# Kernel optimization log

Hardware: AMD Instinct MI355X
Metric: run time of the kernel (lower is better)

The kernel has to match this reference:

```python
import jax, jax.numpy as jnp
import numpy as np

L, D, H, EXP = 6, 512, 8, 4
DH = D // H
EPS = 1e-3  # keras LayerNormalization default epsilon


def _layer_norm(x, gamma, beta):
    mu = jnp.mean(x, axis=-1, keepdims=True)
    var = jnp.mean(jnp.square(x - mu), axis=-1, keepdims=True)
    return (x - mu) * jax.lax.rsqrt(var + EPS) * gamma + beta


def setup_inputs() -> dict:
    key = jax.random.key(0)
    ks = jax.random.split(key, 10)
    B, S = 8, 1024
    s_attn = 1.0 / np.sqrt(D)
    s_ffn1 = 1.0 / np.sqrt(D)
    s_ffn2 = 1.0 / np.sqrt(D * EXP)
    return {
        "x": jax.random.normal(ks[0], (B, S, D), dtype=jnp.float32),
        "Wq": jax.random.normal(ks[1], (L, D, D), dtype=jnp.float32) * s_attn,
        "Wk": jax.random.normal(ks[2], (L, D, D), dtype=jnp.float32) * s_attn,
        "Wv": jax.random.normal(ks[3], (L, D, D), dtype=jnp.float32) * s_attn,
        "Wo": jax.random.normal(ks[4], (L, D, D), dtype=jnp.float32) * s_attn,
        "W1": jax.random.normal(ks[5], (L, D, D * EXP), dtype=jnp.float32) * s_ffn1,
        "b1": jnp.zeros((L, D * EXP), dtype=jnp.float32),
        "W2": jax.random.normal(ks[6], (L, D * EXP, D), dtype=jnp.float32) * s_ffn2,
        "b2": jnp.zeros((L, D), dtype=jnp.float32),
        "g_attn": jnp.ones((L, D), dtype=jnp.float32),
        "be_attn": jnp.zeros((L, D), dtype=jnp.float32),
        "g_ffn": jnp.ones((L, D), dtype=jnp.float32),
        "be_ffn": jnp.zeros((L, D), dtype=jnp.float32),
    }


def _self_attention(y, wq, wk, wv, wo):
    B, S, _ = y.shape
    q = (y @ wq).reshape(B, S, H, DH)
    k = (y @ wk).reshape(B, S, H, DH)
    v = (y @ wv).reshape(B, S, H, DH)
    scores = jnp.einsum("bqhd,bkhd->bhqk", q, k) / np.sqrt(float(DH))
    attn = jax.nn.softmax(scores, axis=-1)
    z = jnp.einsum("bhqk,bkhd->bqhd", attn, v).reshape(B, S, D)
    return z @ wo


def reference(x, Wq, Wk, Wv, Wo, W1, b1, W2, b2, g_attn, be_attn, g_ffn, be_ffn):
    encoded = x
    for l in range(L):
        # pre-LN self-attention + residual (dropout=identity at inference)
        attended = _layer_norm(encoded, g_attn[l], be_attn[l])
        attended = _self_attention(attended, Wq[l], Wk[l], Wv[l], Wo[l])
        attended = encoded + attended
        # pre-LN FFN + residual
        h = _layer_norm(attended, g_ffn[l], be_ffn[l])
        h = jax.nn.relu(h @ W1[l] + b1[l]) @ W2[l] + b2[l]
        encoded = attended + h
    return encoded
```

## Files before the change

### kernel.cpp

```cpp
#include <hip/hip_runtime.h>


#define SEQ 1024
#define ROWS 8192
#define QKVW 1536

using bf16x8 = __attribute__((ext_vector_type(8))) short;
using f32x4  = __attribute__((ext_vector_type(4))) float;

__device__ __forceinline__ unsigned short f2bf(float f) {
  union { float f; unsigned u; } v; v.f = f;
  unsigned r = v.u + 0x7FFFu + ((v.u >> 16) & 1u);
  return (unsigned short)(r >> 16);
}

__device__ __forceinline__ float exp2_fast(float x) {
  float r;
  asm("v_exp_f32 %0, %1" : "=v"(r) : "v"(x));
  return r;
}

__device__ __forceinline__ void gl16(const void* g, void* l) {
  typedef const unsigned int __attribute__((address_space(1)))* GP;
  typedef unsigned int __attribute__((address_space(3)))* LP;
  __builtin_amdgcn_global_load_lds((GP)g, (LP)l, 16, 0, 0);
}

__global__ __launch_bounds__(256) void transpose_cast_k(
    const float* __restrict__ W, unsigned short* __restrict__ Wt,
    int K, int N, int lstride, float scale)
{
  __shared__ float tile[32][33];
  const int l = blockIdx.z;
  const float* Wl = W + (size_t)l * K * N;
  unsigned short* Wtl = Wt + (size_t)l * lstride;
  const int k0 = blockIdx.y * 32, n0 = blockIdx.x * 32;
  const int tx = threadIdx.x & 31, ty = threadIdx.x >> 5;
  #pragma unroll
  for (int i = ty; i < 32; i += 8)
    tile[i][tx] = Wl[(size_t)(k0 + i) * N + n0 + tx];
  __syncthreads();
  #pragma unroll
  for (int i = ty; i < 32; i += 8)
    Wtl[(size_t)(n0 + i) * K + k0 + tx] = f2bf(tile[tx][i] * scale);
}

__global__ __launch_bounds__(256) void ln_k(
    const float* __restrict__ x, const float* __restrict__ g,
    const float* __restrict__ be, unsigned short* __restrict__ y, int rows)
{
  const int wid = (blockIdx.x << 2) | (threadIdx.x >> 6);
  const int lane = threadIdx.x & 63;
  if (wid >= rows) return;
  const float4* xr = reinterpret_cast<const float4*>(x + (size_t)wid * 512);
  float4 a = xr[lane];
  float4 b = xr[lane + 64];
  float s = a.x + a.y + a.z + a.w + b.x + b.y + b.z + b.w;
  #pragma unroll
  for (int m = 32; m >= 1; m >>= 1) s += __shfl_xor(s, m);
  const float mu = s * (1.0f / 512.0f);
  const float d0 = a.x - mu, d1 = a.y - mu, d2 = a.z - mu, d3 = a.w - mu;
  const float e0 = b.x - mu, e1 = b.y - mu, e2 = b.z - mu, e3 = b.w - mu;
  float q = d0*d0 + d1*d1 + d2*d2 + d3*d3 + e0*e0 + e1*e1 + e2*e2 + e3*e3;
  #pragma unroll
  for (int m = 32; m >= 1; m >>= 1) q += __shfl_xor(q, m);
  const float inv = rsqrtf(q * (1.0f / 512.0f) + 1e-3f);
  const float4* gr = reinterpret_cast<const float4*>(g);
  const float4* br = reinterpret_cast<const float4*>(be);
  const float4 g0 = gr[lane], g1 = gr[lane + 64];
  const float4 h0 = br[lane], h1 = br[lane + 64];
  ushort4 o0, o1;
  o0.x = f2bf(d0 * inv * g0.x + h0.x);
  o0.y = f2bf(d1 * inv * g0.y + h0.y);
  o0.z = f2bf(d2 * inv * g0.z + h0.z);
  o0.w = f2bf(d3 * inv * g0.w + h0.w);
  o1.x = f2bf(e0 * inv * g1.x + h1.x);
  o1.y = f2bf(e1 * inv * g1.y + h1.y);
  o1.z = f2bf(e2 * inv * g1.z + h1.z);
  o1.w = f2bf(e3 * inv * g1.w + h1.w);
  *reinterpret_cast<ushort4*>(y + (size_t)wid * 512 + lane * 4) = o0;
  *reinterpret_cast<ushort4*>(y + (size_t)wid * 512 + (lane + 64) * 4) = o1;
}

template<bool RELU, bool HASBIAS, bool HASRES, bool OUTBF>
__global__ __launch_bounds__(256) void gemm128_k(
    const unsigned short* __restrict__ A,
    const unsigned short* __restrict__ Wt,
    const float* __restrict__ bias,
    const float* __restrict__ res,
    void* __restrict__ outp, int M, int N, int K)
{
  __shared__ __align__(16) unsigned short As0[4096], Bs0[4096];
  __shared__ __align__(16) unsigned short As1[4096], Bs1[4096];
  const int t = threadIdx.x;
  const int nwg = gridDim.x * gridDim.y;
  const int bid = blockIdx.y * gridDim.x + blockIdx.x;
  const int nid = (bid & 7) * (nwg >> 3) + (bid >> 3);
  const int bx = nid % gridDim.x, by = nid / gridDim.x;
  const int m0 = by * 128, n0 = bx * 128;
  const int w = t >> 6, lane = t & 63, llo = lane & 15, lhi = lane >> 4;
  const int wr = w >> 1, wc = w & 1;

  const int sr = t >> 2, sg = (t & 3) ^ ((t >> 3) & 3);
  const unsigned short* pa = &A[(size_t)(m0 + sr) * K + sg * 8];
  const unsigned short* pb = &Wt[(size_t)(n0 + sr) * K + sg * 8];

#define GSTAGE128(AsX, BsX, koff) do { \
    gl16(pa + (koff), &AsX[t * 8]); \
    gl16(pa + (size_t)64 * K + (koff), &AsX[2048 + t * 8]); \
    gl16(pb + (koff), &BsX[t * 8]); \
    gl16(pb + (size_t)64 * K + (koff), &BsX[2048 + t * 8]); \
  } while (0)

  const int pgo = (lhi ^ ((llo >> 1) & 3)) * 8;

#define GCOMP128(AsX, BsX) do { \
    bf16x8 af[4], bfr[4]; \
    _Pragma("unroll") \
    for (int f = 0; f < 4; f++) { \
      af[f]  = *reinterpret_cast<const bf16x8*>(&AsX[(wr * 64 + f * 16 + llo) * 32 + pgo]); \
      bfr[f] = *reinterpret_cast<const bf16x8*>(&BsX[(wc * 64 + f * 16 + llo) * 32 + pgo]); \
    } \
    _Pragma("unroll") \
    for (int fi = 0; fi < 4; fi++) \
      _Pragma("unroll") \
      for (int fj = 0; fj < 4; fj++) \
        acc[fi][fj] = __builtin_amdgcn_mfma_f32_16x16x32_bf16(af[fi], bfr[fj], acc[fi][fj], 0, 0, 0); \
  } while (0)

  f32x4 acc[4][4] = {};
  GSTAGE128(As0, Bs0, 0);
  for (int k0 = 0; k0 < K; k0 += 64) {
    __syncthreads();
    GSTAGE128(As1, Bs1, k0 + 32);
    GCOMP128(As0, Bs0);
    __syncthreads();
    if (k0 + 64 < K) GSTAGE128(As0, Bs0, k0 + 64);
    GCOMP128(As1, Bs1);
  }
#undef GSTAGE128
#undef GCOMP128

  const int row0 = m0 + wr * 64, col0 = n0 + wc * 64;
  #pragma unroll
  for (int fi = 0; fi < 4; fi++)
    #pragma unroll
    for (int fj = 0; fj < 4; fj++)
      #pragma unroll
      for (int i = 0; i < 4; i++) {
        const int row = row0 + fi * 16 + lhi * 4 + i;
        const int col = col0 + fj * 16 + llo;
        float v = acc[fi][fj][i];
        if (HASBIAS) v += bias[col];
        if (HASRES)  v += res[(size_t)row * N + col];
        if (RELU)    v = fmaxf(v, 0.0f);
        if (OUTBF) ((unsigned short*)outp)[(size_t)row * N + col] = f2bf(v);
        else       ((float*)outp)[(size_t)row * N + col] = v;
      }
}

template<bool RELU, bool HASBIAS, bool HASRES, bool OUTBF>
__global__ __launch_bounds__(256) void gemm64_k(
    const unsigned short* __restrict__ A,
    const unsigned short* __restrict__ Wt,
    const float* __restrict__ bias,
    const float* __restrict__ res,
    void* __restrict__ outp, int M, int N, int K)
{
  __shared__ __align__(16) unsigned short As0[2048], Bs0[4096];
  __shared__ __align__(16) unsigned short As1[2048], Bs1[4096];
  const int t = threadIdx.x;
  const int nwg = gridDim.x * gridDim.y;
  const int bid = blockIdx.y * gridDim.x + blockIdx.x;
  const int nid = (bid & 7) * (nwg >> 3) + (bid >> 3);
  const int bx = nid % gridDim.x, by = nid / gridDim.x;
  const int m0 = by * 64, n0 = bx * 128;
  const int w = t >> 6, lane = t & 63, llo = lane & 15, lhi = lane >> 4;
  const int wr = w >> 1, wc = w & 1;

  const int sr = t >> 2, sg = (t & 3) ^ ((t >> 3) & 3);
  const unsigned short* pa = &A[(size_t)(m0 + sr) * K + sg * 8];
  const unsigned short* pb = &Wt[(size_t)(n0 + sr) * K + sg * 8];

#define GSTAGE64(AsX, BsX, koff) do { \
    gl16(pa + (koff), &AsX[t * 8]); \
    gl16(pb + (koff), &BsX[t * 8]); \
    gl16(pb + (size_t)64 * K + (koff), &BsX[2048 + t * 8]); \
  } while (0)

  const int pgo = (lhi ^ ((llo >> 1) & 3)) * 8;

#define GCOMP64(AsX, BsX) do { \
    bf16x8 af[2], bfr[4]; \
    _Pragma("unroll") \
    for (int f = 0; f < 2; f++) \
      af[f] = *reinterpret_cast<const bf16x8*>(&AsX[(wr * 32 + f * 16 + llo) * 32 + pgo]); \
    _Pragma("unroll") \
    for (int f = 0; f < 4; f++) \
      bfr[f] = *reinterpret_cast<const bf16x8*>(&BsX[(wc * 64 + f * 16 + llo) * 32 + pgo]); \
    _Pragma("unroll") \
    for (int fi = 0; fi < 2; fi++) \
      _Pragma("unroll") \
      for (int fj = 0; fj < 4; fj++) \
        acc[fi][fj] = __builtin_amdgcn_mfma_f32_16x16x32_bf16(af[fi], bfr[fj], acc[fi][fj], 0, 0, 0); \
  } while (0)

  f32x4 acc[2][4] = {};
  GSTAGE64(As0, Bs0, 0);
  for (int k0 = 0; k0 < K; k0 += 64) {
    __syncthreads();
    GSTAGE64(As1, Bs1, k0 + 32);
    GCOMP64(As0, Bs0);
    __syncthreads();
    if (k0 + 64 < K) GSTAGE64(As0, Bs0, k0 + 64);
    GCOMP64(As1, Bs1);
  }
#undef GSTAGE64
#undef GCOMP64

  const int row0 = m0 + wr * 32, col0 = n0 + wc * 64;
  #pragma unroll
  for (int fi = 0; fi < 2; fi++)
    #pragma unroll
    for (int fj = 0; fj < 4; fj++)
      #pragma unroll
      for (int i = 0; i < 4; i++) {
        const int row = row0 + fi * 16 + lhi * 4 + i;
        const int col = col0 + fj * 16 + llo;
        float v = acc[fi][fj][i];
        if (HASBIAS) v += bias[col];
        if (HASRES)  v += res[(size_t)row * N + col];
        if (RELU)    v = fmaxf(v, 0.0f);
        if (OUTBF) ((unsigned short*)outp)[(size_t)row * N + col] = f2bf(v);
        else       ((float*)outp)[(size_t)row * N + col] = v;
      }
}

__global__ __launch_bounds__(256) void vtrans_k(
    const unsigned short* __restrict__ QKV, unsigned short* __restrict__ VT)
{
  __shared__ unsigned short tile[64][66];
  const int kt = blockIdx.x, bh = blockIdx.y;
  const int bb = bh >> 3, h = bh & 7;
  const int t = threadIdx.x;
  const int r = t >> 2, c0 = (t & 3) * 16;
  const unsigned short* src = &QKV[((size_t)bb * SEQ + kt * 64 + r) * QKVW + 1024 + h * 64 + c0];
  *reinterpret_cast<uint4*>(&tile[r][c0])     = *reinterpret_cast<const uint4*>(src);
  *reinterpret_cast<uint4*>(&tile[r][c0 + 8]) = *reinterpret_cast<const uint4*>(src + 8);
  __syncthreads();
  const int dv = t >> 2, kv0 = (t & 3) * 16;
  unsigned short tmp[16];
  #pragma unroll
  for (int j = 0; j < 16; j++) tmp[j] = tile[kv0 + j][dv];
  ushort4 o0, o1, o2, o3;
  o0.x = tmp[0];  o0.y = tmp[1];  o0.z = tmp[2];  o0.w = tmp[3];
  o1.x = tmp[4];  o1.y = tmp[5];  o1.z = tmp[6];  o1.w = tmp[7];
  o2.x = tmp[8];  o2.y = tmp[9];  o2.z = tmp[10]; o2.w = tmp[11];
  o3.x = tmp[12]; o3.y = tmp[13]; o3.z = tmp[14]; o3.w = tmp[15];
  unsigned short* dst = &VT[((size_t)bh * 64 + dv) * SEQ + kt * 64 + kv0];
  *reinterpret_cast<ushort4*>(dst)      = o0;
  *reinterpret_cast<ushort4*>(dst + 4)  = o1;
  *reinterpret_cast<ushort4*>(dst + 8)  = o2;
  *reinterpret_cast<ushort4*>(dst + 12) = o3;
}

__global__ __launch_bounds__(256) void attn_k(
    const unsigned short* __restrict__ QKV,
    const unsigned short* __restrict__ VT,
    unsigned short* __restrict__ Zb)
{
  __shared__ __align__(16) unsigned short Ks0[4096], Vs0[4096];
  __shared__ __align__(16) unsigned short Ks1[4096], Vs1[4096];
  __shared__ __align__(16) unsigned short Ps[4096];

  const int t = threadIdx.x;
  const int qt = blockIdx.x, h = blockIdx.y, bb = blockIdx.z;
  const int w = t >> 6, lane = t & 63, llo = lane & 15, lhi = lane >> 4;
  const size_t rowb = (size_t)bb * SEQ;
  const int kcol = 512 + h * 64;
  const size_t vtb = (size_t)(bb * 8 + h) * 64 * SEQ;

  bf16x8 aq[2];
  #pragma unroll
  for (int ds = 0; ds < 2; ds++)
    aq[ds] = *reinterpret_cast<const bf16x8*>(
        &QKV[(rowb + qt * 64 + w * 16 + llo) * QKVW + h * 64 + ds * 32 + lhi * 8]);

  const int cA = t, cB = 256 + t;
  const int gA = cA >> 6, lA = cA & 63, gB = cB >> 6, lB = cB & 63;
  const unsigned short* kpA = &QKV[(rowb + (gA >> 1) * 16 + (lA & 15)) * QKVW + kcol + (gA & 1) * 32 + (lA >> 4) * 8];
  const unsigned short* kpB = &QKV[(rowb + (gB >> 1) * 16 + (lB & 15)) * QKVW + kcol + (gB & 1) * 32 + (lB >> 4) * 8];
  const unsigned short* vpA = &VT[vtb + (size_t)((gA >> 1) * 16 + (lA & 15)) * SEQ + (gA & 1) * 32 + (lA >> 4) * 8];
  const unsigned short* vpB = &VT[vtb + (size_t)((gB >> 1) * 16 + (lB & 15)) * SEQ + (gB & 1) * 32 + (lB >> 4) * 8];

#define ASTAGE(KsX, VsX, ktt) do { \
    gl16(kpA + (size_t)(ktt) * 64 * QKVW, &KsX[cA * 8]); \
    gl16(kpB + (size_t)(ktt) * 64 * QKVW, &KsX[cB * 8]); \
    gl16(vpA + (ktt) * 64, &VsX[cA * 8]); \
    gl16(vpB + (ktt) * 64, &VsX[cB * 8]); \
  } while (0)

#define ACOMP(KsX, VsX) do { \
    f32x4 s_[4]; \
    _Pragma("unroll") \
    for (int fj = 0; fj < 4; fj++) \
      _Pragma("unroll") \
      for (int i = 0; i < 4; i++) s_[fj][i] = -16.0f; \
    _Pragma("unroll") \
    for (int ds = 0; ds < 2; ds++) \
      _Pragma("unroll") \
      for (int fj = 0; fj < 4; fj++) { \
        bf16x8 bk = *reinterpret_cast<const bf16x8*>(&KsX[((fj * 2 + ds) * 64 + lane) * 8]); \
        s_[fj] = __builtin_amdgcn_mfma_f32_16x16x32_bf16(aq[ds], bk, s_[fj], 0, 0, 0); \
      } \
    _Pragma("unroll") \
    for (int fj = 0; fj < 4; fj++) \
      _Pragma("unroll") \
      for (int i = 0; i < 4; i++) { \
        const float p = exp2_fast(s_[fj][i]); \
        l_[i] += p; \
        Ps[w * 1024 + (fj >> 1) * 512 + ((fj & 1) * 2 + (llo >> 3)) * 128 \
           + (lhi * 4 + i) * 8 + (llo & 7)] = f2bf(p); \
      } \
    _Pragma("unroll") \
    for (int ks = 0; ks < 2; ks++) { \
      bf16x8 ap = *reinterpret_cast<const bf16x8*>(&Ps[w * 1024 + (ks * 64 + lane) * 8]); \
      _Pragma("unroll") \
      for (int fo = 0; fo < 4; fo++) { \
        bf16x8 bv = *reinterpret_cast<const bf16x8*>(&VsX[((fo * 2 + ks) * 64 + lane) * 8]); \
        o_[fo] = __builtin_amdgcn_mfma_f32_16x16x32_bf16(ap, bv, o_[fo], 0, 0, 0); \
      } \
    } \
  } while (0)

  float l_[4] = {0.0f, 0.0f, 0.0f, 0.0f};
  f32x4 o_[4] = {};

  ASTAGE(Ks0, Vs0, 0);
  for (int kt = 0; kt < 16; kt += 2) {
    __syncthreads();
    ASTAGE(Ks1, Vs1, kt + 1);
    ACOMP(Ks0, Vs0);
    __syncthreads();
    if (kt + 2 < 16) ASTAGE(Ks0, Vs0, kt + 2);
    ACOMP(Ks1, Vs1);
  }
#undef ASTAGE
#undef ACOMP

  #pragma unroll
  for (int i = 0; i < 4; i++) {
    l_[i] += __shfl_xor(l_[i], 1);
    l_[i] += __shfl_xor(l_[i], 2);
    l_[i] += __shfl_xor(l_[i], 4);
    l_[i] += __shfl_xor(l_[i], 8);
  }

  #pragma unroll
  for (int fo = 0; fo < 4; fo++)
    #pragma unroll
    for (int i = 0; i < 4; i++) {
      const float v = o_[fo][i] / l_[i];
      Zb[(rowb + qt * 64 + w * 16 + lhi * 4 + i) * 512 + h * 64 + fo * 16 + llo] = f2bf(v);
    }
}

extern "C" void kernel_launch(void* const* d_in, const int* in_sizes, int n_in,
                              void* d_out, int out_size, void* d_ws, size_t ws_size,
                              hipStream_t stream)
{
  const float* x   = (const float*)d_in[0];
  const float* Wq  = (const float*)d_in[1];
  const float* Wk  = (const float*)d_in[2];
  const float* Wv  = (const float*)d_in[3];
  const float* Wo  = (const float*)d_in[4];
  const float* W1  = (const float*)d_in[5];
  const float* b1  = (const float*)d_in[6];
  const float* W2  = (const float*)d_in[7];
  const float* b2  = (const float*)d_in[8];
  const float* ga  = (const float*)d_in[9];
  const float* ba  = (const float*)d_in[10];
  const float* gf  = (const float*)d_in[11];
  const float* bfn = (const float*)d_in[12];
  float* out = (float*)d_out;

  char* p = (char*)d_ws;
  auto alloc = [&](size_t bytes) { void* r = (void*)p; p += (bytes + 255) & ~(size_t)255; return r; };
  float* E0 = (float*)alloc((size_t)ROWS * 512 * 4);
  float* E1 = (float*)alloc((size_t)ROWS * 512 * 4);
  unsigned short* Ybf   = (unsigned short*)alloc((size_t)ROWS * 512 * 2);
  unsigned short* QKVbf = (unsigned short*)alloc((size_t)ROWS * QKVW * 2);
  unsigned short* H1bf  = (unsigned short*)alloc((size_t)ROWS * 2048 * 2);
  unsigned short* VT    = H1bf;
  unsigned short* WtQKV = (unsigned short*)alloc(6ull * QKVW * 512 * 2);
  unsigned short* WtO   = (unsigned short*)alloc(6ull * 512 * 512 * 2);
  unsigned short* Wt1   = (unsigned short*)alloc(6ull * 2048 * 512 * 2);
  unsigned short* Wt2   = (unsigned short*)alloc(6ull * 512 * 2048 * 2);
  unsigned short* Zbf   = Ybf;

  const float qscale = 0.125f * 1.44269504f;
  transpose_cast_k<<<dim3(16, 16, 6), 256, 0, stream>>>(Wq, WtQKV,          512, 512,  QKVW * 512, qscale);
  transpose_cast_k<<<dim3(16, 16, 6), 256, 0, stream>>>(Wk, WtQKV + 262144, 512, 512,  QKVW * 512, 1.0f);
  transpose_cast_k<<<dim3(16, 16, 6), 256, 0, stream>>>(Wv, WtQKV + 524288, 512, 512,  QKVW * 512, 1.0f);
  transpose_cast_k<<<dim3(16, 16, 6), 256, 0, stream>>>(Wo, WtO,            512, 512,  262144,     1.0f);
  transpose_cast_k<<<dim3(64, 16, 6), 256, 0, stream>>>(W1, Wt1,            512, 2048, 1048576,    1.0f);
  transpose_cast_k<<<dim3(16, 64, 6), 256, 0, stream>>>(W2, Wt2,            2048, 512, 1048576,    1.0f);

  for (int l = 0; l < 6; l++) {
    const float* enc = (l == 0) ? x : E0;
    ln_k<<<2048, 256, 0, stream>>>(enc, ga + l * 512, ba + l * 512, Ybf, ROWS);
    gemm128_k<false, false, false, true><<<dim3(12, 64), 256, 0, stream>>>(
        Ybf, WtQKV + (size_t)l * QKVW * 512, nullptr, nullptr, QKVbf, ROWS, QKVW, 512);
    vtrans_k<<<dim3(16, 64), 256, 0, stream>>>(QKVbf, VT);
    attn_k<<<dim3(16, 8, 8), 256, 0, stream>>>(QKVbf, VT, Zbf);
    gemm64_k<false, false, true, false><<<dim3(4, 128), 256, 0, stream>>>(
        Zbf, WtO + (size_t)l * 262144, nullptr, enc, E1, ROWS, 512, 512);
    ln_k<<<2048, 256, 0, stream>>>(E1, gf + l * 512, bfn + l * 512, Ybf, ROWS);
    gemm128_k<true, true, false, true><<<dim3(16, 64), 256, 0, stream>>>(
        Ybf, Wt1 + (size_t)l * 1048576, b1 + l * 2048, nullptr, H1bf, ROWS, 2048, 512);
    gemm64_k<false, true, true, false><<<dim3(4, 128), 256, 0, stream>>>(
        H1bf, Wt2 + (size_t)l * 1048576, b2 + l * 512, E1, (l == 5) ? out : E0,
        ROWS, 512, 2048);
  }
}
```

Measured before the change: 904.6 us.

## Load K/V fragments directly from global into registers, swizzle P, remap grid

The attention kernel no longer stages K and V tiles through double-buffered shared memory with barriers. Each wave now loads its MFMA operand fragments for K and V straight from global memory (L2) into registers every iteration. It also XOR-swizzles the per-wave P scratch buffer to avoid LDS bank conflicts, and linearizes the grid with a remap that groups query tiles of the same batch-head onto neighbouring blocks for cache locality. This removes the barriers and the LDS traffic, at the cost of each of the four waves redundantly fetching the same K/V data from global and losing the prefetch overlap.

```diff
diff --git a/kernel.cpp b/kernel.cpp
--- a/kernel.cpp
+++ b/kernel.cpp
@@ -269,16 +269,17 @@
     const unsigned short* __restrict__ VT,
     unsigned short* __restrict__ Zb)
 {
-  __shared__ __align__(16) unsigned short Ks0[4096], Vs0[4096];
-  __shared__ __align__(16) unsigned short Ks1[4096], Vs1[4096];
   __shared__ __align__(16) unsigned short Ps[4096];
 
   const int t = threadIdx.x;
-  const int qt = blockIdx.x, h = blockIdx.y, bb = blockIdx.z;
+  const int n = blockIdx.x;
+  const int m = n >> 3;
+  const int g = (n & 7) + 8 * (m >> 4);
+  const int qt = m & 15;
+  const int h = g & 7, bb = g >> 3;
   const int w = t >> 6, lane = t & 63, llo = lane & 15, lhi = lane >> 4;
   const size_t rowb = (size_t)bb * SEQ;
-  const int kcol = 512 + h * 64;
-  const size_t vtb = (size_t)(bb * 8 + h) * 64 * SEQ;
+  const size_t vtb = (size_t)g * 64 * SEQ;
 
   bf16x8 aq[2];
   #pragma unroll
@@ -286,67 +287,62 @@
     aq[ds] = *reinterpret_cast<const bf16x8*>(
         &QKV[(rowb + qt * 64 + w * 16 + llo) * QKVW + h * 64 + ds * 32 + lhi * 8]);
 
-  const int cA = t, cB = 256 + t;
-  const int gA = cA >> 6, lA = cA & 63, gB = cB >> 6, lB = cB & 63;
-  const unsigned short* kpA = &QKV[(rowb + (gA >> 1) * 16 + (lA & 15)) * QKVW + kcol + (gA & 1) * 32 + (lA >> 4) * 8];
-  const unsigned short* kpB = &QKV[(rowb + (gB >> 1) * 16 + (lB & 15)) * QKVW + kcol + (gB & 1) * 32 + (lB >> 4) * 8];
-  const unsigned short* vpA = &VT[vtb + (size_t)((gA >> 1) * 16 + (lA & 15)) * SEQ + (gA & 1) * 32 + (lA >> 4) * 8];
-  const unsigned short* vpB = &VT[vtb + (size_t)((gB >> 1) * 16 + (lB & 15)) * SEQ + (gB & 1) * 32 + (lB >> 4) * 8];
-
-#define ASTAGE(KsX, VsX, ktt) do { \
-    gl16(kpA + (size_t)(ktt) * 64 * QKVW, &KsX[cA * 8]); \
-    gl16(kpB + (size_t)(ktt) * 64 * QKVW, &KsX[cB * 8]); \
-    gl16(vpA + (ktt) * 64, &VsX[cA * 8]); \
-    gl16(vpB + (ktt) * 64, &VsX[cB * 8]); \
-  } while (0)
-
-#define ACOMP(KsX, VsX) do { \
-    f32x4 s_[4]; \
-    _Pragma("unroll") \
-    for (int fj = 0; fj < 4; fj++) \
-      _Pragma("unroll") \
-      for (int i = 0; i < 4; i++) s_[fj][i] = -16.0f; \
-    _Pragma("unroll") \
-    for (int ds = 0; ds < 2; ds++) \
-      _Pragma("unroll") \
-      for (int fj = 0; fj < 4; fj++) { \
-        bf16x8 bk = *reinterpret_cast<const bf16x8*>(&KsX[((fj * 2 + ds) * 64 + lane) * 8]); \
-        s_[fj] = __builtin_amdgcn_mfma_f32_16x16x32_bf16(aq[ds], bk, s_[fj], 0, 0, 0); \
-      } \
-    _Pragma("unroll") \
-    for (int fj = 0; fj < 4; fj++) \
-      _Pragma("unroll") \
-      for (int i = 0; i < 4; i++) { \
-        const float p = exp2_fast(s_[fj][i]); \
-        l_[i] += p; \
-        Ps[w * 1024 + (fj >> 1) * 512 + ((fj & 1) * 2 + (llo >> 3)) * 128 \
-           + (lhi * 4 + i) * 8 + (llo & 7)] = f2bf(p); \
-      } \
-    _Pragma("unroll") \
-    for (int ks = 0; ks < 2; ks++) { \
-      bf16x8 ap = *reinterpret_cast<const bf16x8*>(&Ps[w * 1024 + (ks * 64 + lane) * 8]); \
-      _Pragma("unroll") \
-      for (int fo = 0; fo < 4; fo++) { \
-        bf16x8 bv = *reinterpret_cast<const bf16x8*>(&VsX[((fo * 2 + ks) * 64 + lane) * 8]); \
-        o_[fo] = __builtin_amdgcn_mfma_f32_16x16x32_bf16(ap, bv, o_[fo], 0, 0, 0); \
-      } \
-    } \
-  } while (0)
+  const unsigned short* kR[4];
+  const unsigned short* vR[4];
+  #pragma unroll
+  for (int f = 0; f < 4; f++) {
+    kR[f] = &QKV[(rowb + f * 16 + llo) * QKVW + 512 + h * 64 + lhi * 8];
+    vR[f] = &VT[vtb + (size_t)(f * 16 + llo) * SEQ + lhi * 8];
+  }
+
+  const int pwr = w * 1024;
+  const int prd = (lane ^ ((lane >> 2) & 3)) * 8;
+  const int wgb = ((llo >> 3)) * 16;
 
   float l_[4] = {0.0f, 0.0f, 0.0f, 0.0f};
   f32x4 o_[4] = {};
 
-  ASTAGE(Ks0, Vs0, 0);
-  for (int kt = 0; kt < 16; kt += 2) {
-    __syncthreads();
-    ASTAGE(Ks1, Vs1, kt + 1);
-    ACOMP(Ks0, Vs0);
-    __syncthreads();
-    if (kt + 2 < 16) ASTAGE(Ks0, Vs0, kt + 2);
-    ACOMP(Ks1, Vs1);
-  }
-#undef ASTAGE
-#undef ACOMP
+  for (int kt = 0; kt < 16; kt++) {
+    const int ko = kt * 64;
+    bf16x8 bk[2][4], bv[2][4];
+    #pragma unroll
+    for (int ds = 0; ds < 2; ds++)
+      #pragma unroll
+      for (int f = 0; f < 4; f++) {
+        bk[ds][f] = *reinterpret_cast<const bf16x8*>(kR[f] + (size_t)ko * QKVW + ds * 32);
+        bv[ds][f] = *reinterpret_cast<const bf16x8*>(vR[f] + ko + ds * 32);
+      }
+
+    f32x4 s_[4];
+    #pragma unroll
+    for (int fj = 0; fj < 4; fj++)
+      #pragma unroll
+      for (int i = 0; i < 4; i++) s_[fj][i] = -16.0f;
+    #pragma unroll
+    for (int ds = 0; ds < 2; ds++)
+      #pragma unroll
+      for (int fj = 0; fj < 4; fj++)
+        s_[fj] = __builtin_amdgcn_mfma_f32_16x16x32_bf16(aq[ds], bk[ds][fj], s_[fj], 0, 0, 0);
+
+    #pragma unroll
+    for (int fj = 0; fj < 4; fj++)
+      #pragma unroll
+      for (int i = 0; i < 4; i++) {
+        const float p = exp2_fast(s_[fj][i]);
+        l_[i] += p;
+        const int gsub = ((fj & 1) * 2) * 16 + wgb + lhi * 4 + i;
+        const int phys = gsub ^ lhi;
+        Ps[pwr + (fj >> 1) * 512 + phys * 8 + (llo & 7)] = f2bf(p);
+      }
+
+    #pragma unroll
+    for (int ks = 0; ks < 2; ks++) {
+      bf16x8 ap = *reinterpret_cast<const bf16x8*>(&Ps[pwr + ks * 512 + prd]);
+      #pragma unroll
+      for (int fo = 0; fo < 4; fo++)
+        o_[fo] = __builtin_amdgcn_mfma_f32_16x16x32_bf16(ap, bv[ks][fo], o_[fo], 0, 0, 0);
+    }
+  }
 
   #pragma unroll
   for (int i = 0; i < 4; i++) {
@@ -412,7 +408,7 @@
     gemm128_k<false, false, false, true><<<dim3(12, 64), 256, 0, stream>>>(
         Ybf, WtQKV + (size_t)l * QKVW * 512, nullptr, nullptr, QKVbf, ROWS, QKVW, 512);
     vtrans_k<<<dim3(16, 64), 256, 0, stream>>>(QKVbf, VT);
-    attn_k<<<dim3(16, 8, 8), 256, 0, stream>>>(QKVbf, VT, Zbf);
+    attn_k<<<dim3(1024), 256, 0, stream>>>(QKVbf, VT, Zbf);
     gemm64_k<false, false, true, false><<<dim3(4, 128), 256, 0, stream>>>(
         Zbf, WtO + (size_t)l * 262144, nullptr, enc, E1, ROWS, 512, 512);
     ln_k<<<2048, 256, 0, stream>>>(E1, gf + l * 512, bfn + l * 512, Ybf, ROWS);
```

Result: slower. 1.347 ms (+48.9%).
